# Kernel tuning notes

Measured on AMD Instinct MI355X. Metric: run time of the kernel, lower is better.

Reference implementation:

```python
import jax, jax.numpy as jnp
import numpy as np

N_ATOMS = 100000
N_EDGES = 300000
ATOM_DIM = 32
BOND_DIM = 16
STEPS = 4


def setup_inputs() -> dict:
    key = jax.random.key(0)
    ks = jax.random.split(key, 8)
    atom_features = jax.random.normal(ks[0], (N_ATOMS, ATOM_DIM), dtype=jnp.float32)
    bond_features = jax.random.normal(ks[1], (N_EDGES, BOND_DIM), dtype=jnp.float32)
    pair_indices = jax.random.randint(ks[2], (N_EDGES, 2), 0, N_ATOMS, dtype=jnp.int64 if jax.config.jax_enable_x64 else jnp.int32)
    W_bond = jax.random.normal(ks[3], (BOND_DIM, ATOM_DIM * ATOM_DIM), dtype=jnp.float32) * 0.05
    b_bond = jnp.zeros((ATOM_DIM * ATOM_DIM,), dtype=jnp.float32)
    W_ih = jax.random.normal(ks[4], (3 * ATOM_DIM, ATOM_DIM), dtype=jnp.float32) * 0.1
    W_hh = jax.random.normal(ks[5], (3 * ATOM_DIM, ATOM_DIM), dtype=jnp.float32) * 0.1
    b_ih = jnp.zeros((3 * ATOM_DIM,), dtype=jnp.float32)
    b_hh = jnp.zeros((3 * ATOM_DIM,), dtype=jnp.float32)
    return {
        'atom_features': atom_features,
        'bond_features': bond_features,
        'pair_indices': pair_indices,
        'W_bond': W_bond, 'b_bond': b_bond,
        'W_ih': W_ih, 'W_hh': W_hh, 'b_ih': b_ih, 'b_hh': b_hh,
    }


def _gru_cell(x, h, W_ih, W_hh, b_ih, b_hh):
    # torch.nn.GRUCell semantics
    gi = x @ W_ih.T + b_ih  # [N, 3H]
    gh = h @ W_hh.T + b_hh
    i_r, i_z, i_n = jnp.split(gi, 3, axis=-1)
    h_r, h_z, h_n = jnp.split(gh, 3, axis=-1)
    r = jax.nn.sigmoid(i_r + h_r)
    z = jax.nn.sigmoid(i_z + h_z)
    n = jnp.tanh(i_n + r * h_n)
    return (1.0 - z) * n + z * h


def reference(atom_features, bond_features, pair_indices, W_bond, b_bond, W_ih, W_hh, b_ih, b_hh):
    n_atoms, d = atom_features.shape
    # Edge transform matrices (identical every step in the original; hoisted)
    edge_mats = (bond_features @ W_bond + b_bond).reshape(-1, d, d)  # [E, d, d]
    dst = pair_indices[:, 0]
    nbr = pair_indices[:, 1]
    h = atom_features
    for _ in range(STEPS):
        # gather neighbor states, per-edge matvec, scatter-add
        msg = jnp.einsum('eij,ej->ei', edge_mats, h[nbr])  # [E, d]
        agg = jax.ops.segment_sum(msg, dst, num_segments=n_atoms)  # [N, d]
        h = _gru_cell(agg, h, W_ih, W_hh, b_ih, b_hh)
    return h
```

## Files before the change

### kernel.cpp

```cpp
#include <hip/hip_runtime.h>

#define NA 100000
#define NE 300000
#define STEPS 4
#define NTILES (NE / 16)
#define ATILES (NA / 16)

typedef _Float16 f16;
typedef _Float16 half8 __attribute__((ext_vector_type(8)));
using f32x4 = __attribute__((ext_vector_type(4))) float;

__global__ __launch_bounds__(256) void zero_kernel(float4* __restrict__ p, int n4)
{
    int t = blockIdx.x * 256 + threadIdx.x;
    if (t < n4) p[t] = make_float4(0.f, 0.f, 0.f, 0.f);
}

__global__ __launch_bounds__(256) void conv_kernel(
    const float* __restrict__ src, f16* __restrict__ dst, int n8)
{
    int t = blockIdx.x * 256 + threadIdx.x;
    if (t >= n8) return;
    float4 a = reinterpret_cast<const float4*>(src)[2 * t];
    float4 b = reinterpret_cast<const float4*>(src)[2 * t + 1];
    half8 o;
    o[0]=(f16)a.x; o[1]=(f16)a.y; o[2]=(f16)a.z; o[3]=(f16)a.w;
    o[4]=(f16)b.x; o[5]=(f16)b.y; o[6]=(f16)b.z; o[7]=(f16)b.w;
    reinterpret_cast<half8*>(dst)[t] = o;
}

__global__ __launch_bounds__(256) void prep_kernel(
    const float* __restrict__ Wb, const float* __restrict__ bb,
    const float* __restrict__ Wih, const float* __restrict__ Whh,
    f16* __restrict__ Wbt, f16* __restrict__ Wihb, f16* __restrict__ Whhb)
{
    int t = blockIdx.x * 256 + threadIdx.x;
    if (t < 17 * 32 * 32) {
        int j = t & 31, i = (t >> 5) & 31, k = t >> 10;
        float v = (k < 16) ? Wb[k * 1024 + i * 32 + j] : bb[i * 32 + j];
        int row = ((i & 4) ? 16 : 0) + ((i >> 3) << 2) + (i & 3);
        Wbt[(k * 32 + row) * 32 + j] = (f16)v;
    } else if (t < 17 * 32 * 32 + 3072) {
        int u = t - 17 * 32 * 32;
        Wihb[u] = (f16)Wih[u];
    } else if (t < 17 * 32 * 32 + 6144) {
        int u = t - 17 * 32 * 32 - 3072;
        Whhb[u] = (f16)Whh[u];
    }
}

__global__ __launch_bounds__(256) void hist_kernel(
    const int* __restrict__ pair, int* __restrict__ cnt)
{
    int e = blockIdx.x * 256 + threadIdx.x;
    if (e < NE) atomicAdd(&cnt[reinterpret_cast<const int2*>(pair)[e].x], 1);
}

__global__ __launch_bounds__(1024) void scan1_kernel(
    const int* __restrict__ cnt, int* __restrict__ excl, int* __restrict__ bsum)
{
    __shared__ int tmp[1024];
    int g = blockIdx.x * 1024 + threadIdx.x;
    int v = (g < NA) ? cnt[g] : 0;
    tmp[threadIdx.x] = v;
    __syncthreads();
    for (int off = 1; off < 1024; off <<= 1) {
        int u = (threadIdx.x >= off) ? tmp[threadIdx.x - off] : 0;
        __syncthreads();
        tmp[threadIdx.x] += u;
        __syncthreads();
    }
    if (g < NA) excl[g] = tmp[threadIdx.x] - v;
    if (threadIdx.x == 1023) bsum[blockIdx.x] = tmp[1023];
}

__global__ __launch_bounds__(128) void scan2_kernel(int* __restrict__ bsum, int nb)
{
    __shared__ int tmp[128];
    int i = threadIdx.x;
    int v = (i < nb) ? bsum[i] : 0;
    tmp[i] = v;
    __syncthreads();
    for (int off = 1; off < 128; off <<= 1) {
        int u = (i >= off) ? tmp[i - off] : 0;
        __syncthreads();
        tmp[i] += u;
        __syncthreads();
    }
    if (i < nb) bsum[i] = tmp[i] - v;
}

__global__ __launch_bounds__(256) void scan3_kernel(
    const int* __restrict__ excl, const int* __restrict__ bsum,
    int* __restrict__ rowptr, int* __restrict__ next)
{
    int g = blockIdx.x * 256 + threadIdx.x;
    if (g < NA) {
        int v = excl[g] + bsum[g >> 10];
        rowptr[g] = v;
        next[g] = v;
    }
    if (g == NA) rowptr[NA] = NE;
}

__global__ __launch_bounds__(256) void scatter_kernel(
    const float* __restrict__ bond, const int* __restrict__ pair,
    int* __restrict__ next, int* __restrict__ nbrp, f16* __restrict__ bondp)
{
    int e = blockIdx.x * 256 + threadIdx.x;
    if (e >= NE) return;
    int2 p = reinterpret_cast<const int2*>(pair)[e];
    int pos = atomicAdd(&next[p.x], 1);
    nbrp[pos] = p.y;
    const float4* b4 = reinterpret_cast<const float4*>(bond + (size_t)e * 16);
    float4 b0 = b4[0], b1 = b4[1], b2 = b4[2], b3 = b4[3];
    half8 o0, o1;
    o0[0]=(f16)b0.x; o0[1]=(f16)b0.y; o0[2]=(f16)b0.z; o0[3]=(f16)b0.w;
    o0[4]=(f16)b1.x; o0[5]=(f16)b1.y; o0[6]=(f16)b1.z; o0[7]=(f16)b1.w;
    o1[0]=(f16)b2.x; o1[1]=(f16)b2.y; o1[2]=(f16)b2.z; o1[3]=(f16)b2.w;
    o1[4]=(f16)b3.x; o1[5]=(f16)b3.y; o1[6]=(f16)b3.z; o1[7]=(f16)b3.w;
    half8* dst = reinterpret_cast<half8*>(bondp + (size_t)pos * 16);
    dst[0] = o0; dst[1] = o1;
}

__global__ __launch_bounds__(256, 2) void msg_kernel(
    const f16* __restrict__ hb,
    const f16* __restrict__ bondp,
    const int* __restrict__ nbrp,
    const f16* __restrict__ Wbt,
    f16* __restrict__ msg)
{
    int wave = threadIdx.x >> 6;
    int lane = threadIdx.x & 63;
    int col  = lane & 15;
    int kg   = lane >> 4;

    half8 w0[17], w1[17];
#pragma unroll
    for (int s = 0; s < 17; ++s) {
        w0[s] = *reinterpret_cast<const half8*>(Wbt + (s * 32 + col) * 32 + kg * 8);
        w1[s] = *reinterpret_cast<const half8*>(Wbt + (s * 32 + 16 + col) * 32 + kg * 8);
    }

    int wid = blockIdx.x * 4 + wave;
    int nw  = gridDim.x << 2;

    int tile = wid;
    if (tile >= NTILES) return;

    int pos = tile * 16 + col;
    int nbr0 = nbrp[pos];
    half8 cA = *reinterpret_cast<const half8*>(bondp + (size_t)pos * 16);
    half8 cB = *reinterpret_cast<const half8*>(bondp + (size_t)pos * 16 + 8);
    half8 hf = *reinterpret_cast<const half8*>(hb + (size_t)nbr0 * 32 + kg * 8);

    int tileN = tile + nw;
    int nbrN = 0;
    if (tileN < NTILES) nbrN = nbrp[tileN * 16 + col];

    while (tile < NTILES) {
        half8 hf2{}, cA2{}, cB2{};
        if (tileN < NTILES) {
            int posN = tileN * 16 + col;
            cA2 = *reinterpret_cast<const half8*>(bondp + (size_t)posN * 16);
            cB2 = *reinterpret_cast<const half8*>(bondp + (size_t)posN * 16 + 8);
            hf2 = *reinterpret_cast<const half8*>(hb + (size_t)nbrN * 32 + kg * 8);
        }
        int tileNN = tileN + nw;
        int nbrNN = 0;
        if (tileNN < NTILES) nbrNN = nbrp[tileNN * 16 + col];

        f32x4 acc0 = {0.f, 0.f, 0.f, 0.f};
        f32x4 acc1 = {0.f, 0.f, 0.f, 0.f};
#pragma unroll
        for (int s = 0; s < 16; ++s) {
            f16 ch = (s < 8) ? cA[s] : cB[s - 8];
            half8 a = hf * ch;
            acc0 = __builtin_amdgcn_mfma_f32_16x16x32_f16(w0[s], a, acc0, 0, 0, 0);
            acc1 = __builtin_amdgcn_mfma_f32_16x16x32_f16(w1[s], a, acc1, 0, 0, 0);
        }
        acc0 = __builtin_amdgcn_mfma_f32_16x16x32_f16(w0[16], hf, acc0, 0, 0, 0);
        acc1 = __builtin_amdgcn_mfma_f32_16x16x32_f16(w1[16], hf, acc1, 0, 0, 0);

        half8 so;
        so[0]=(f16)acc0[0]; so[1]=(f16)acc0[1]; so[2]=(f16)acc0[2]; so[3]=(f16)acc0[3];
        so[4]=(f16)acc1[0]; so[5]=(f16)acc1[1]; so[6]=(f16)acc1[2]; so[7]=(f16)acc1[3];
        *reinterpret_cast<half8*>(msg + (size_t)pos * 32 + kg * 8) = so;

        pos = tileN * 16 + col;
        tile = tileN; tileN = tileNN;
        hf = hf2; cA = cA2; cB = cB2; nbrN = nbrNN;
    }
}

__global__ __launch_bounds__(256) void gru_kernel(
    const f16* __restrict__ msg,
    const int* __restrict__ rowptr,
    const f16* __restrict__ hb,
    const f16* __restrict__ Wihb,
    const f16* __restrict__ Whhb,
    const float* __restrict__ bih, const float* __restrict__ bhh,
    float* __restrict__ hout, f16* __restrict__ hbf, int write_f32)
{
    int wave = threadIdx.x >> 6;
    int lane = threadIdx.x & 63;
    int tile = blockIdx.x * 4 + wave;
    if (tile >= ATILES) return;

    int base = tile * 16;
    int col  = lane & 15;
    int kg   = lane >> 4;
    int a0   = base + col;

    int st = rowptr[a0], en = rowptr[a0 + 1];
    half8 hfrag = *reinterpret_cast<const half8*>(hb + (size_t)a0 * 32 + kg * 8);

    half8 wi[6], wh[6];
#pragma unroll
    for (int t = 0; t < 6; ++t) {
        wi[t] = *reinterpret_cast<const half8*>(Wihb + (size_t)(t * 16 + col) * 32 + kg * 8);
        wh[t] = *reinterpret_cast<const half8*>(Whhb + (size_t)(t * 16 + col) * 32 + kg * 8);
    }
    float br0  = bih[col]      + bhh[col];
    float bz0  = bih[32 + col] + bhh[32 + col];
    float bin0 = bih[64 + col];
    float bhn0 = bhh[64 + col];
    float br1  = bih[16 + col]      + bhh[16 + col];
    float bz1  = bih[48 + col] + bhh[48 + col];
    float bin1 = bih[80 + col];
    float bhn1 = bhh[80 + col];

    float xs[8] = {0.f, 0.f, 0.f, 0.f, 0.f, 0.f, 0.f, 0.f};
    int p = st;
    while (p < en) {
        int n = en - p;
        half8 m0, m1, m2, m3;
        m0 = *reinterpret_cast<const half8*>(msg + (size_t)p * 32 + kg * 8);
        if (n > 1) m1 = *reinterpret_cast<const half8*>(msg + (size_t)(p + 1) * 32 + kg * 8);
        if (n > 2) m2 = *reinterpret_cast<const half8*>(msg + (size_t)(p + 2) * 32 + kg * 8);
        if (n > 3) m3 = *reinterpret_cast<const half8*>(msg + (size_t)(p + 3) * 32 + kg * 8);
#pragma unroll
        for (int j = 0; j < 8; ++j) xs[j] += (float)m0[j];
        if (n > 1) {
#pragma unroll
            for (int j = 0; j < 8; ++j) xs[j] += (float)m1[j];
        }
        if (n > 2) {
#pragma unroll
            for (int j = 0; j < 8; ++j) xs[j] += (float)m2[j];
        }
        if (n > 3) {
#pragma unroll
            for (int j = 0; j < 8; ++j) xs[j] += (float)m3[j];
        }
        p += 4;
    }
    half8 xfrag;
#pragma unroll
    for (int j = 0; j < 8; ++j) xfrag[j] = (f16)xs[j];

    f32x4 gi[6], gh[6];
#pragma unroll
    for (int t = 0; t < 6; ++t) {
        f32x4 z = {0.f, 0.f, 0.f, 0.f};
        gi[t] = __builtin_amdgcn_mfma_f32_16x16x32_f16(xfrag, wi[t], z, 0, 0, 0);
        gh[t] = __builtin_amdgcn_mfma_f32_16x16x32_f16(hfrag, wh[t], z, 0, 0, 0);
    }

#pragma unroll
    for (int hh = 0; hh < 2; ++hh) {
        float br  = hh ? br1  : br0;
        float bz  = hh ? bz1  : bz0;
        float bin = hh ? bin1 : bin0;
        float bhn = hh ? bhn1 : bhn0;
        int i = hh * 16 + col;
#pragma unroll
        for (int reg = 0; reg < 4; ++reg) {
            int a = base + kg * 4 + reg;
            float r = 1.f / (1.f + __expf(-(gi[hh][reg] + gh[hh][reg] + br)));
            float z = 1.f / (1.f + __expf(-(gi[2 + hh][reg] + gh[2 + hh][reg] + bz)));
            float n = tanhf(gi[4 + hh][reg] + bin + r * (gh[4 + hh][reg] + bhn));
            float hp = (float)hb[(size_t)a * 32 + i];
            float o  = (1.f - z) * n + z * hp;
            if (write_f32) hout[(size_t)a * 32 + i] = o;
            hbf[(size_t)a * 32 + i] = (f16)o;
        }
    }
}

extern "C" void kernel_launch(void* const* d_in, const int* in_sizes, int n_in,
                              void* d_out, int out_size, void* d_ws, size_t ws_size,
                              hipStream_t stream)
{
    const float* atom = (const float*)d_in[0];
    const float* bond = (const float*)d_in[1];
    const int*   pair = (const int*)  d_in[2];
    const float* Wb   = (const float*)d_in[3];
    const float* bb   = (const float*)d_in[4];
    const float* W_ih = (const float*)d_in[5];
    const float* W_hh = (const float*)d_in[6];
    const float* b_ih = (const float*)d_in[7];
    const float* b_hh = (const float*)d_in[8];
    float* out = (float*)d_out;

    char* w = (char*)d_ws;
    f16* msg    = (f16*)w;
    f16* hbf    = (f16*)(w + 19200000);
    f16* bondp  = (f16*)(w + 25600000);
    f16* Wbt    = (f16*)(w + 35200000);
    f16* Wihb   = Wbt + 17 * 32 * 32;
    f16* Whhb   = Wihb + 96 * 32;
    int* rowcnt = (int*)(w + 35248000);
    int* excl   = (int*)(w + 35648000);
    int* bsum   = (int*)(w + 36048000);
    int* rowptr = (int*)(w + 36048512);
    int* next   = (int*)(w + 36448516);
    int* nbrp   = (int*)(w + 36848516);

    const int nsb = (NA + 1023) / 1024;

    zero_kernel<<<(NA * 4 / 16 + 255) / 256, 256, 0, stream>>>((float4*)rowcnt, NA * 4 / 16);
    hist_kernel<<<(NE + 255) / 256, 256, 0, stream>>>(pair, rowcnt);
    scan1_kernel<<<nsb, 1024, 0, stream>>>(rowcnt, excl, bsum);
    scan2_kernel<<<1, 128, 0, stream>>>(bsum, nsb);
    scan3_kernel<<<(NA + 1 + 255) / 256, 256, 0, stream>>>(excl, bsum, rowptr, next);
    scatter_kernel<<<(NE + 255) / 256, 256, 0, stream>>>(bond, pair, next, nbrp, bondp);

    prep_kernel<<<(17 * 32 * 32 + 6144 + 255) / 256, 256, 0, stream>>>(
        Wb, bb, W_ih, W_hh, Wbt, Wihb, Whhb);
    conv_kernel<<<(NA * 32 / 8 + 255) / 256, 256, 0, stream>>>(atom, hbf, NA * 32 / 8);

    const int gru_blocks = (ATILES + 3) / 4;
    for (int s = 0; s < STEPS; ++s) {
        msg_kernel<<<512, 256, 0, stream>>>(hbf, bondp, nbrp, Wbt, msg);
        gru_kernel<<<gru_blocks, 256, 0, stream>>>(msg, rowptr, hbf, Wihb, Whhb,
                                                   b_ih, b_hh, out, hbf,
                                                   (s == STEPS - 1) ? 1 : 0);
    }
}
```

Baseline: 203.8 us.

## Fuse message-passing steps into a persistent cooperative kernel with grid sync

```diff
diff --git a/kernel.cpp b/kernel.cpp
--- a/kernel.cpp
+++ b/kernel.cpp
@@ -1,51 +1,56 @@
 #include <hip/hip_runtime.h>
+#include <hip/hip_cooperative_groups.h>
+
+namespace cg = cooperative_groups;
 
 #define NA 100000
 #define NE 300000
 #define STEPS 4
 #define NTILES (NE / 16)
 #define ATILES (NA / 16)
+#define GBLK 512
 
 typedef _Float16 f16;
 typedef _Float16 half8 __attribute__((ext_vector_type(8)));
 using f32x4 = __attribute__((ext_vector_type(4))) float;
 
-__global__ __launch_bounds__(256) void zero_kernel(float4* __restrict__ p, int n4)
-{
-    int t = blockIdx.x * 256 + threadIdx.x;
-    if (t < n4) p[t] = make_float4(0.f, 0.f, 0.f, 0.f);
-}
-
-__global__ __launch_bounds__(256) void conv_kernel(
-    const float* __restrict__ src, f16* __restrict__ dst, int n8)
-{
-    int t = blockIdx.x * 256 + threadIdx.x;
-    if (t >= n8) return;
-    float4 a = reinterpret_cast<const float4*>(src)[2 * t];
-    float4 b = reinterpret_cast<const float4*>(src)[2 * t + 1];
-    half8 o;
-    o[0]=(f16)a.x; o[1]=(f16)a.y; o[2]=(f16)a.z; o[3]=(f16)a.w;
-    o[4]=(f16)b.x; o[5]=(f16)b.y; o[6]=(f16)b.z; o[7]=(f16)b.w;
-    reinterpret_cast<half8*>(dst)[t] = o;
-}
-
-__global__ __launch_bounds__(256) void prep_kernel(
+__global__ __launch_bounds__(256) void setup_kernel(
+    const float* __restrict__ atom,
     const float* __restrict__ Wb, const float* __restrict__ bb,
     const float* __restrict__ Wih, const float* __restrict__ Whh,
-    f16* __restrict__ Wbt, f16* __restrict__ Wihb, f16* __restrict__ Whhb)
+    f16* __restrict__ hbf, f16* __restrict__ Wbt,
+    f16* __restrict__ Wihb, f16* __restrict__ Whhb,
+    int* __restrict__ rowcnt, int* __restrict__ total)
 {
     int t = blockIdx.x * 256 + threadIdx.x;
-    if (t < 17 * 32 * 32) {
-        int j = t & 31, i = (t >> 5) & 31, k = t >> 10;
-        float v = (k < 16) ? Wb[k * 1024 + i * 32 + j] : bb[i * 32 + j];
+    const int NH8 = NA * 32 / 8;
+    if (t < NH8) {
+        float4 a = reinterpret_cast<const float4*>(atom)[2 * t];
+        float4 b = reinterpret_cast<const float4*>(atom)[2 * t + 1];
+        half8 o;
+        o[0]=(f16)a.x; o[1]=(f16)a.y; o[2]=(f16)a.z; o[3]=(f16)a.w;
+        o[4]=(f16)b.x; o[5]=(f16)b.y; o[6]=(f16)b.z; o[7]=(f16)b.w;
+        reinterpret_cast<half8*>(hbf)[t] = o;
+        return;
+    }
+    int u = t - NH8;
+    if (u < NA) {
+        rowcnt[u] = 0;
+        if (u == 0) *total = 0;
+        return;
+    }
+    int v = u - NA;
+    if (v < 17 * 32 * 32) {
+        int j = v & 31, i = (v >> 5) & 31, k = v >> 10;
+        float val = (k < 16) ? Wb[k * 1024 + i * 32 + j] : bb[i * 32 + j];
         int row = ((i & 4) ? 16 : 0) + ((i >> 3) << 2) + (i & 3);
-        Wbt[(k * 32 + row) * 32 + j] = (f16)v;
-    } else if (t < 17 * 32 * 32 + 3072) {
-        int u = t - 17 * 32 * 32;
-        Wihb[u] = (f16)Wih[u];
-    } else if (t < 17 * 32 * 32 + 6144) {
-        int u = t - 17 * 32 * 32 - 3072;
-        Whhb[u] = (f16)Whh[u];
+        Wbt[(k * 32 + row) * 32 + j] = (f16)val;
+    } else if (v < 17 * 32 * 32 + 3072) {
+        int q = v - 17 * 32 * 32;
+        Wihb[q] = (f16)Wih[q];
+    } else if (v < 17 * 32 * 32 + 6144) {
+        int q = v - 17 * 32 * 32 - 3072;
+        Whhb[q] = (f16)Whh[q];
     }
 }
 
@@ -56,10 +61,12 @@
     if (e < NE) atomicAdd(&cnt[reinterpret_cast<const int2*>(pair)[e].x], 1);
 }
 
-__global__ __launch_bounds__(1024) void scan1_kernel(
-    const int* __restrict__ cnt, int* __restrict__ excl, int* __restrict__ bsum)
+__global__ __launch_bounds__(1024) void alloc_kernel(
+    const int* __restrict__ cnt, int* __restrict__ start,
+    int* __restrict__ next, int* __restrict__ total)
 {
     __shared__ int tmp[1024];
+    __shared__ int base;
     int g = blockIdx.x * 1024 + threadIdx.x;
     int v = (g < NA) ? cnt[g] : 0;
     tmp[threadIdx.x] = v;
@@ -70,37 +77,13 @@
         tmp[threadIdx.x] += u;
         __syncthreads();
     }
-    if (g < NA) excl[g] = tmp[threadIdx.x] - v;
-    if (threadIdx.x == 1023) bsum[blockIdx.x] = tmp[1023];
-}
-
-__global__ __launch_bounds__(128) void scan2_kernel(int* __restrict__ bsum, int nb)
-{
-    __shared__ int tmp[128];
-    int i = threadIdx.x;
-    int v = (i < nb) ? bsum[i] : 0;
-    tmp[i] = v;
+    if (threadIdx.x == 1023) base = atomicAdd(total, tmp[1023]);
     __syncthreads();
-    for (int off = 1; off < 128; off <<= 1) {
-        int u = (i >= off) ? tmp[i - off] : 0;
-        __syncthreads();
-        tmp[i] += u;
-        __syncthreads();
-    }
-    if (i < nb) bsum[i] = tmp[i] - v;
-}
-
-__global__ __launch_bounds__(256) void scan3_kernel(
-    const int* __restrict__ excl, const int* __restrict__ bsum,
-    int* __restrict__ rowptr, int* __restrict__ next)
-{
-    int g = blockIdx.x * 256 + threadIdx.x;
     if (g < NA) {
-        int v = excl[g] + bsum[g >> 10];
-        rowptr[g] = v;
-        next[g] = v;
-    }
-    if (g == NA) rowptr[NA] = NE;
+        int s = base + tmp[threadIdx.x] - v;
+        start[g] = s;
+        next[g] = s;
+    }
 }
 
 __global__ __launch_bounds__(256) void scatter_kernel(
@@ -123,168 +106,193 @@
     dst[0] = o0; dst[1] = o1;
 }
 
+__device__ __forceinline__ void msg_body(
+    const f16* __restrict__ h, const f16* __restrict__ bondp,
+    const int* __restrict__ nbrp, const f16* __restrict__ Wbt,
+    f16* __restrict__ msgb, int wid, int nw, int col, int kg)
+{
+    half8 w0[17], w1[17];
+#pragma unroll
+    for (int t = 0; t < 17; ++t) {
+        w0[t] = *reinterpret_cast<const half8*>(Wbt + (t * 32 + col) * 32 + kg * 8);
+        w1[t] = *reinterpret_cast<const half8*>(Wbt + (t * 32 + 16 + col) * 32 + kg * 8);
+    }
+    int tile = wid;
+    int pos = 0;
+    half8 hf{}, cA{}, cB{};
+    if (tile < NTILES) {
+        pos = tile * 16 + col;
+        int nbr0 = nbrp[pos];
+        cA = *reinterpret_cast<const half8*>(bondp + (size_t)pos * 16);
+        cB = *reinterpret_cast<const half8*>(bondp + (size_t)pos * 16 + 8);
+        hf = *reinterpret_cast<const half8*>(h + (size_t)nbr0 * 32 + kg * 8);
+    }
+    while (tile < NTILES) {
+        int tile2 = tile + nw;
+        int pos2 = 0;
+        half8 hf2{}, cA2{}, cB2{};
+        if (tile2 < NTILES) {
+            pos2 = tile2 * 16 + col;
+            int nbr2 = nbrp[pos2];
+            cA2 = *reinterpret_cast<const half8*>(bondp + (size_t)pos2 * 16);
+            cB2 = *reinterpret_cast<const half8*>(bondp + (size_t)pos2 * 16 + 8);
+            hf2 = *reinterpret_cast<const half8*>(h + (size_t)nbr2 * 32 + kg * 8);
+        }
+        f32x4 acc0 = {0.f, 0.f, 0.f, 0.f};
+        f32x4 acc1 = {0.f, 0.f, 0.f, 0.f};
+#pragma unroll
+        for (int t = 0; t < 16; ++t) {
+            f16 ch = (t < 8) ? cA[t] : cB[t - 8];
+            half8 a = hf * ch;
+            acc0 = __builtin_amdgcn_mfma_f32_16x16x32_f16(w0[t], a, acc0, 0, 0, 0);
+            acc1 = __builtin_amdgcn_mfma_f32_16x16x32_f16(w1[t], a, acc1, 0, 0, 0);
+        }
+        acc0 = __builtin_amdgcn_mfma_f32_16x16x32_f16(w0[16], hf, acc0, 0, 0, 0);
+        acc1 = __builtin_amdgcn_mfma_f32_16x16x32_f16(w1[16], hf, acc1, 0, 0, 0);
+
+        half8 so;
+        so[0]=(f16)acc0[0]; so[1]=(f16)acc0[1]; so[2]=(f16)acc0[2]; so[3]=(f16)acc0[3];
+        so[4]=(f16)acc1[0]; so[5]=(f16)acc1[1]; so[6]=(f16)acc1[2]; so[7]=(f16)acc1[3];
+        *reinterpret_cast<half8*>(msgb + (size_t)pos * 32 + kg * 8) = so;
+
+        tile = tile2; pos = pos2; hf = hf2; cA = cA2; cB = cB2;
+    }
+}
+
+__device__ __forceinline__ void gru_body(
+    const f16* __restrict__ msgb, const int* __restrict__ start,
+    const int* __restrict__ cnt, f16* __restrict__ h,
+    const f16* __restrict__ Wihb, const f16* __restrict__ Whhb,
+    const float* __restrict__ bih, const float* __restrict__ bhh,
+    float* __restrict__ hout, int wf, int wid, int nw, int col, int kg)
+{
+    half8 wi[6], wh[6];
+#pragma unroll
+    for (int t = 0; t < 6; ++t) {
+        wi[t] = *reinterpret_cast<const half8*>(Wihb + (size_t)(t * 16 + col) * 32 + kg * 8);
+        wh[t] = *reinterpret_cast<const half8*>(Whhb + (size_t)(t * 16 + col) * 32 + kg * 8);
+    }
+    float br0  = bih[col]      + bhh[col];
+    float bz0  = bih[32 + col] + bhh[32 + col];
+    float bin0 = bih[64 + col];
+    float bhn0 = bhh[64 + col];
+    float br1  = bih[16 + col] + bhh[16 + col];
+    float bz1  = bih[48 + col] + bhh[48 + col];
+    float bin1 = bih[80 + col];
+    float bhn1 = bhh[80 + col];
+
+    for (int tile = wid; tile < ATILES; tile += nw) {
+        int base = tile * 16;
+        int a0   = base + col;
+        int st = start[a0], en = st + cnt[a0];
+        half8 hfrag = *reinterpret_cast<const half8*>(h + (size_t)a0 * 32 + kg * 8);
+
+        float xs[8] = {0.f, 0.f, 0.f, 0.f, 0.f, 0.f, 0.f, 0.f};
+        int p = st;
+        while (p < en) {
+            int n = en - p;
+            half8 m0, m1, m2, m3;
+            m0 = *reinterpret_cast<const half8*>(msgb + (size_t)p * 32 + kg * 8);
+            if (n > 1) m1 = *reinterpret_cast<const half8*>(msgb + (size_t)(p + 1) * 32 + kg * 8);
+            if (n > 2) m2 = *reinterpret_cast<const half8*>(msgb + (size_t)(p + 2) * 32 + kg * 8);
+            if (n > 3) m3 = *reinterpret_cast<const half8*>(msgb + (size_t)(p + 3) * 32 + kg * 8);
+#pragma unroll
+            for (int j = 0; j < 8; ++j) xs[j] += (float)m0[j];
+            if (n > 1) {
+#pragma unroll
+                for (int j = 0; j < 8; ++j) xs[j] += (float)m1[j];
+            }
+            if (n > 2) {
+#pragma unroll
+                for (int j = 0; j < 8; ++j) xs[j] += (float)m2[j];
+            }
+            if (n > 3) {
+#pragma unroll
+                for (int j = 0; j < 8; ++j) xs[j] += (float)m3[j];
+            }
+            p += 4;
+        }
+        half8 xfrag;
+#pragma unroll
+        for (int j = 0; j < 8; ++j) xfrag[j] = (f16)xs[j];
+
+        f32x4 gi[6], gh[6];
+#pragma unroll
+        for (int t = 0; t < 6; ++t) {
+            f32x4 z = {0.f, 0.f, 0.f, 0.f};
+            gi[t] = __builtin_amdgcn_mfma_f32_16x16x32_f16(xfrag, wi[t], z, 0, 0, 0);
+            gh[t] = __builtin_amdgcn_mfma_f32_16x16x32_f16(hfrag, wh[t], z, 0, 0, 0);
+        }
+
+#pragma unroll
+        for (int hh = 0; hh < 2; ++hh) {
+            float br  = hh ? br1  : br0;
+            float bz  = hh ? bz1  : bz0;
+            float bin = hh ? bin1 : bin0;
+            float bhn = hh ? bhn1 : bhn0;
+            int i = hh * 16 + col;
+#pragma unroll
+            for (int reg = 0; reg < 4; ++reg) {
+                int a = base + kg * 4 + reg;
+                float r = 1.f / (1.f + __expf(-(gi[hh][reg] + gh[hh][reg] + br)));
+                float z = 1.f / (1.f + __expf(-(gi[2 + hh][reg] + gh[2 + hh][reg] + bz)));
+                float n = tanhf(gi[4 + hh][reg] + bin + r * (gh[4 + hh][reg] + bhn));
+                float hp = (float)h[(size_t)a * 32 + i];
+                float o  = (1.f - z) * n + z * hp;
+                if (wf) hout[(size_t)a * 32 + i] = o;
+                h[(size_t)a * 32 + i] = (f16)o;
+            }
+        }
+    }
+}
+
 __global__ __launch_bounds__(256, 2) void msg_kernel(
-    const f16* __restrict__ hb,
-    const f16* __restrict__ bondp,
-    const int* __restrict__ nbrp,
-    const f16* __restrict__ Wbt,
-    f16* __restrict__ msg)
-{
+    const f16* __restrict__ hb, const f16* __restrict__ bondp,
+    const int* __restrict__ nbrp, const f16* __restrict__ Wbt,
+    f16* __restrict__ msgb)
+{
+    int wave = threadIdx.x >> 6;
+    int lane = threadIdx.x & 63;
+    msg_body(hb, bondp, nbrp, Wbt, msgb,
+             blockIdx.x * 4 + wave, gridDim.x << 2, lane & 15, lane >> 4);
+}
+
+__global__ __launch_bounds__(256) void gru_kernel(
+    const f16* __restrict__ msgb, const int* __restrict__ start,
+    const int* __restrict__ cnt, f16* __restrict__ hb,
+    const f16* __restrict__ Wihb, const f16* __restrict__ Whhb,
+    const float* __restrict__ bih, const float* __restrict__ bhh,
+    float* __restrict__ hout, int wf)
+{
+    int wave = threadIdx.x >> 6;
+    int lane = threadIdx.x & 63;
+    gru_body(msgb, start, cnt, hb, Wihb, Whhb, bih, bhh, hout, wf,
+             blockIdx.x * 4 + wave, gridDim.x << 2, lane & 15, lane >> 4);
+}
+
+__global__ __launch_bounds__(256, 2) void step_kernel(
+    f16* __restrict__ h, const f16* __restrict__ bondp,
+    const int* __restrict__ nbrp, const f16* __restrict__ Wbt,
+    f16* __restrict__ msgb, const int* __restrict__ start,
+    const int* __restrict__ cnt,
+    const f16* __restrict__ Wihb, const f16* __restrict__ Whhb,
+    const float* __restrict__ bih, const float* __restrict__ bhh,
+    float* __restrict__ hout)
+{
+    cg::grid_group grid = cg::this_grid();
     int wave = threadIdx.x >> 6;
     int lane = threadIdx.x & 63;
     int col  = lane & 15;
     int kg   = lane >> 4;
-
-    half8 w0[17], w1[17];
-#pragma unroll
-    for (int s = 0; s < 17; ++s) {
-        w0[s] = *reinterpret_cast<const half8*>(Wbt + (s * 32 + col) * 32 + kg * 8);
-        w1[s] = *reinterpret_cast<const half8*>(Wbt + (s * 32 + 16 + col) * 32 + kg * 8);
-    }
-
-    int wid = blockIdx.x * 4 + wave;
-    int nw  = gridDim.x << 2;
-
-    int tile = wid;
-    if (tile >= NTILES) return;
-
-    int pos = tile * 16 + col;
-    int nbr0 = nbrp[pos];
-    half8 cA = *reinterpret_cast<const half8*>(bondp + (size_t)pos * 16);
-    half8 cB = *reinterpret_cast<const half8*>(bondp + (size_t)pos * 16 + 8);
-    half8 hf = *reinterpret_cast<const half8*>(hb + (size_t)nbr0 * 32 + kg * 8);
-
-    int tileN = tile + nw;
-    int nbrN = 0;
-    if (tileN < NTILES) nbrN = nbrp[tileN * 16 + col];
-
-    while (tile < NTILES) {
-        half8 hf2{}, cA2{}, cB2{};
-        if (tileN < NTILES) {
-            int posN = tileN * 16 + col;
-            cA2 = *reinterpret_cast<const half8*>(bondp + (size_t)posN * 16);
-            cB2 = *reinterpret_cast<const half8*>(bondp + (size_t)posN * 16 + 8);
-            hf2 = *reinterpret_cast<const half8*>(hb + (size_t)nbrN * 32 + kg * 8);
-        }
-        int tileNN = tileN + nw;
-        int nbrNN = 0;
-        if (tileNN < NTILES) nbrNN = nbrp[tileNN * 16 + col];
-
-        f32x4 acc0 = {0.f, 0.f, 0.f, 0.f};
-        f32x4 acc1 = {0.f, 0.f, 0.f, 0.f};
-#pragma unroll
-        for (int s = 0; s < 16; ++s) {
-            f16 ch = (s < 8) ? cA[s] : cB[s - 8];
-            half8 a = hf * ch;
-            acc0 = __builtin_amdgcn_mfma_f32_16x16x32_f16(w0[s], a, acc0, 0, 0, 0);
-            acc1 = __builtin_amdgcn_mfma_f32_16x16x32_f16(w1[s], a, acc1, 0, 0, 0);
-        }
-        acc0 = __builtin_amdgcn_mfma_f32_16x16x32_f16(w0[16], hf, acc0, 0, 0, 0);
-        acc1 = __builtin_amdgcn_mfma_f32_16x16x32_f16(w1[16], hf, acc1, 0, 0, 0);
-
-        half8 so;
-        so[0]=(f16)acc0[0]; so[1]=(f16)acc0[1]; so[2]=(f16)acc0[2]; so[3]=(f16)acc0[3];
-        so[4]=(f16)acc1[0]; so[5]=(f16)acc1[1]; so[6]=(f16)acc1[2]; so[7]=(f16)acc1[3];
-        *reinterpret_cast<half8*>(msg + (size_t)pos * 32 + kg * 8) = so;
-
-        pos = tileN * 16 + col;
-        tile = tileN; tileN = tileNN;
-        hf = hf2; cA = cA2; cB = cB2; nbrN = nbrNN;
-    }
-}
-
-__global__ __launch_bounds__(256) void gru_kernel(
-    const f16* __restrict__ msg,
-    const int* __restrict__ rowptr,
-    const f16* __restrict__ hb,
-    const f16* __restrict__ Wihb,
-    const f16* __restrict__ Whhb,
-    const float* __restrict__ bih, const float* __restrict__ bhh,
-    float* __restrict__ hout, f16* __restrict__ hbf, int write_f32)
-{
-    int wave = threadIdx.x >> 6;
-    int lane = threadIdx.x & 63;
-    int tile = blockIdx.x * 4 + wave;
-    if (tile >= ATILES) return;
-
-    int base = tile * 16;
-    int col  = lane & 15;
-    int kg   = lane >> 4;
-    int a0   = base + col;
-
-    int st = rowptr[a0], en = rowptr[a0 + 1];
-    half8 hfrag = *reinterpret_cast<const half8*>(hb + (size_t)a0 * 32 + kg * 8);
-
-    half8 wi[6], wh[6];
-#pragma unroll
-    for (int t = 0; t < 6; ++t) {
-        wi[t] = *reinterpret_cast<const half8*>(Wihb + (size_t)(t * 16 + col) * 32 + kg * 8);
-        wh[t] = *reinterpret_cast<const half8*>(Whhb + (size_t)(t * 16 + col) * 32 + kg * 8);
-    }
-    float br0  = bih[col]      + bhh[col];
-    float bz0  = bih[32 + col] + bhh[32 + col];
-    float bin0 = bih[64 + col];
-    float bhn0 = bhh[64 + col];
-    float br1  = bih[16 + col]      + bhh[16 + col];
-    float bz1  = bih[48 + col] + bhh[48 + col];
-    float bin1 = bih[80 + col];
-    float bhn1 = bhh[80 + col];
-
-    float xs[8] = {0.f, 0.f, 0.f, 0.f, 0.f, 0.f, 0.f, 0.f};
-    int p = st;
-    while (p < en) {
-        int n = en - p;
-        half8 m0, m1, m2, m3;
-        m0 = *reinterpret_cast<const half8*>(msg + (size_t)p * 32 + kg * 8);
-        if (n > 1) m1 = *reinterpret_cast<const half8*>(msg + (size_t)(p + 1) * 32 + kg * 8);
-        if (n > 2) m2 = *reinterpret_cast<const half8*>(msg + (size_t)(p + 2) * 32 + kg * 8);
-        if (n > 3) m3 = *reinterpret_cast<const half8*>(msg + (size_t)(p + 3) * 32 + kg * 8);
-#pragma unroll
-        for (int j = 0; j < 8; ++j) xs[j] += (float)m0[j];
-        if (n > 1) {
-#pragma unroll
-            for (int j = 0; j < 8; ++j) xs[j] += (float)m1[j];
-        }
-        if (n > 2) {
-#pragma unroll
-            for (int j = 0; j < 8; ++j) xs[j] += (float)m2[j];
-        }
-        if (n > 3) {
-#pragma unroll
-            for (int j = 0; j < 8; ++j) xs[j] += (float)m3[j];
-        }
-        p += 4;
-    }
-    half8 xfrag;
-#pragma unroll
-    for (int j = 0; j < 8; ++j) xfrag[j] = (f16)xs[j];
-
-    f32x4 gi[6], gh[6];
-#pragma unroll
-    for (int t = 0; t < 6; ++t) {
-        f32x4 z = {0.f, 0.f, 0.f, 0.f};
-        gi[t] = __builtin_amdgcn_mfma_f32_16x16x32_f16(xfrag, wi[t], z, 0, 0, 0);
-        gh[t] = __builtin_amdgcn_mfma_f32_16x16x32_f16(hfrag, wh[t], z, 0, 0, 0);
-    }
-
-#pragma unroll
-    for (int hh = 0; hh < 2; ++hh) {
-        float br  = hh ? br1  : br0;
-        float bz  = hh ? bz1  : bz0;
-        float bin = hh ? bin1 : bin0;
-        float bhn = hh ? bhn1 : bhn0;
-        int i = hh * 16 + col;
-#pragma unroll
-        for (int reg = 0; reg < 4; ++reg) {
-            int a = base + kg * 4 + reg;
-            float r = 1.f / (1.f + __expf(-(gi[hh][reg] + gh[hh][reg] + br)));
-            float z = 1.f / (1.f + __expf(-(gi[2 + hh][reg] + gh[2 + hh][reg] + bz)));
-            float n = tanhf(gi[4 + hh][reg] + bin + r * (gh[4 + hh][reg] + bhn));
-            float hp = (float)hb[(size_t)a * 32 + i];
-            float o  = (1.f - z) * n + z * hp;
-            if (write_f32) hout[(size_t)a * 32 + i] = o;
-            hbf[(size_t)a * 32 + i] = (f16)o;
-        }
+    int wid  = blockIdx.x * 4 + wave;
+    int nw   = gridDim.x << 2;
+
+    for (int s = 0; s < STEPS; ++s) {
+        msg_body(h, bondp, nbrp, Wbt, msgb, wid, nw, col, kg);
+        grid.sync();
+        gru_body(msgb, start, cnt, h, Wihb, Whhb, bih, bhh, hout,
+                 (s == STEPS - 1) ? 1 : 0, wid, nw, col, kg);
+        grid.sync();
     }
 }
 
@@ -311,30 +319,36 @@
     f16* Wihb   = Wbt + 17 * 32 * 32;
     f16* Whhb   = Wihb + 96 * 32;
     int* rowcnt = (int*)(w + 35248000);
-    int* excl   = (int*)(w + 35648000);
-    int* bsum   = (int*)(w + 36048000);
-    int* rowptr = (int*)(w + 36048512);
-    int* next   = (int*)(w + 36448516);
-    int* nbrp   = (int*)(w + 36848516);
-
-    const int nsb = (NA + 1023) / 1024;
-
-    zero_kernel<<<(NA * 4 / 16 + 255) / 256, 256, 0, stream>>>((float4*)rowcnt, NA * 4 / 16);
+    int* startp = (int*)(w + 35648000);
+    int* nextp  = (int*)(w + 36048000);
+    int* nbrp   = (int*)(w + 36448000);
+    int* total  = (int*)(w + 37648000);
+
+    const int setup_threads = NA * 32 / 8 + NA + 17 * 32 * 32 + 6144;
+    setup_kernel<<<(setup_threads + 255) / 256, 256, 0, stream>>>(
+        atom, Wb, bb, W_ih, W_hh, hbf, Wbt, Wihb, Whhb, rowcnt, total);
     hist_kernel<<<(NE + 255) / 256, 256, 0, stream>>>(pair, rowcnt);
-    scan1_kernel<<<nsb, 1024, 0, stream>>>(rowcnt, excl, bsum);
-    scan2_kernel<<<1, 128, 0, stream>>>(bsum, nsb);
-    scan3_kernel<<<(NA + 1 + 255) / 256, 256, 0, stream>>>(excl, bsum, rowptr, next);
-    scatter_kernel<<<(NE + 255) / 256, 256, 0, stream>>>(bond, pair, next, nbrp, bondp);
-
-    prep_kernel<<<(17 * 32 * 32 + 6144 + 255) / 256, 256, 0, stream>>>(
-        Wb, bb, W_ih, W_hh, Wbt, Wihb, Whhb);
-    conv_kernel<<<(NA * 32 / 8 + 255) / 256, 256, 0, stream>>>(atom, hbf, NA * 32 / 8);
-
-    const int gru_blocks = (ATILES + 3) / 4;
-    for (int s = 0; s < STEPS; ++s) {
-        msg_kernel<<<512, 256, 0, stream>>>(hbf, bondp, nbrp, Wbt, msg);
-        gru_kernel<<<gru_blocks, 256, 0, stream>>>(msg, rowptr, hbf, Wihb, Whhb,
-                                                   b_ih, b_hh, out, hbf,
-                                                   (s == STEPS - 1) ? 1 : 0);
-    }
-}
+    alloc_kernel<<<(NA + 1023) / 1024, 1024, 0, stream>>>(rowcnt, startp, nextp, total);
+    scatter_kernel<<<(NE + 255) / 256, 256, 0, stream>>>(bond, pair, nextp, nbrp, bondp);
+
+    int bpc = 0;
+    hipError_t qe = hipOccupancyMaxActiveBlocksPerMultiprocessor(
+        &bpc, (const void*)step_kernel, 256, 0);
+    if (qe == hipSuccess && bpc >= 2) {
+        void* args[12];
+        args[0]  = &hbf;   args[1]  = &bondp;  args[2]  = &nbrp;
+        args[3]  = &Wbt;   args[4]  = &msg;    args[5]  = &startp;
+        args[6]  = &rowcnt; args[7] = &Wihb;   args[8]  = &Whhb;
+        args[9]  = (void*)&b_ih; args[10] = (void*)&b_hh; args[11] = &out;
+        hipLaunchCooperativeKernel((void*)step_kernel, dim3(GBLK), dim3(256),
+                                   args, 0, stream);
+    } else {
+        const int gru_blocks = (ATILES + 3) / 4;
+        for (int s = 0; s < STEPS; ++s) {
+            msg_kernel<<<512, 256, 0, stream>>>(hbf, bondp, nbrp, Wbt, msg);
+            gru_kernel<<<gru_blocks, 256, 0, stream>>>(msg, startp, rowcnt, hbf,
+                                                       Wihb, Whhb, b_ih, b_hh, out,
+                                                       (s == STEPS - 1) ? 1 : 0);
+        }
+    }
+}
```

After: 195.3 us. 4.1% less time.
